# Performance work log

Measured on AMD Instinct MI355X. Metric: run time of the kernel, lower is better.

## Reference

```python
import jax, jax.numpy as jnp
from jax import lax
import numpy as np


def _conv3d(x, W, b, stride=1, pad=1):
    y = lax.conv_general_dilated(x, W, (stride,) * 3, [(pad, pad)] * 3,
                                 dimension_numbers=('NCDHW', 'OIDHW', 'NCDHW'))
    return y + b[None, :, None, None, None]


def _deconv3d(x, W, b):
    # PyTorch ConvTranspose3d(k=4, s=2, p=1) == conv with lhs_dilation=2,
    # per-side pad = k-1-p = 2, spatially flipped kernel; W is (Cin, Cout, 4,4,4).
    Wf = jnp.flip(W, axis=(2, 3, 4)).transpose(1, 0, 2, 3, 4)
    y = lax.conv_general_dilated(x, Wf, (1, 1, 1), [(2, 2)] * 3,
                                 lhs_dilation=(2, 2, 2),
                                 dimension_numbers=('NCDHW', 'OIDHW', 'NCDHW'))
    return y + b[None, :, None, None, None]


def _inorm(x, eps=1e-5):
    # InstanceNorm3d (affine=False): normalize per (B, C) over spatial dims
    m = jnp.mean(x, axis=(2, 3, 4), keepdims=True)
    v = jnp.var(x, axis=(2, 3, 4), keepdims=True)
    return (x - m) * lax.rsqrt(v + eps)


def _leaky(x):
    return jnp.where(x >= 0, x, 0.1 * x)


def _cblock(x, W, b, stride=1):
    return _leaky(_inorm(_conv3d(x, W, b, stride)))


def _cost_volume(f1, f2, r=2):
    # Faithful to the original pad/mul/crop loop:
    # cost[shift][p] = mean_c f1[c, p] * f2[c, p + shift], zero-padded OOB.
    B, C, D, H, W = f1.shape
    f2p = jnp.pad(f2, ((0, 0), (0, 0), (r, r), (r, r), (r, r)))
    cv = [jnp.mean(f1 * f2p[:, :, r + v:r + v + D, r + h:r + h + H, r + d:r + d + W], axis=1)
          for v in range(-r, r + 1)
          for h in range(-r, r + 1)
          for d in range(-r, r + 1)]
    return jnp.stack(cv, axis=1)  # (B, (2r+1)^3 = 125, D, H, W)


def _warp(img, flow):
    # SpatialTransformation: dense 3D warp, trilinear sample at grid + flow,
    # coordinates clamped to the volume border.
    B, C, D, H, W = img.shape
    gd, gh, gw = jnp.meshgrid(jnp.arange(D, dtype=img.dtype),
                              jnp.arange(H, dtype=img.dtype),
                              jnp.arange(W, dtype=img.dtype), indexing='ij')
    cd = jnp.clip(gd[None] + flow[:, 0], 0.0, D - 1.0)
    ch = jnp.clip(gh[None] + flow[:, 1], 0.0, H - 1.0)
    cw = jnp.clip(gw[None] + flow[:, 2], 0.0, W - 1.0)

    def samp_b(imb, d, h, w):
        return jax.vmap(lambda c: jax.scipy.ndimage.map_coordinates(
            c, [d, h, w], order=1, mode='nearest'))(imb)

    return jax.vmap(samp_b)(img, cd, ch, cw)


def _forward(atlas, target, W_ct, b_ct, W1a, b1a, W1aa, b1aa, W1b, b1b,
             W2a, b2a, W2aa, b2aa, W2b, b2b,
             W20, b20, Wpf2, bpf2, Wd2, bd2, Wuf2, buf2,
             W10, b10, Wpf1, bpf1, Wd1, bd1, Wuf1, buf1,
             W00, b00, Wpf0, bpf0, Wd0, bd0):
    # modality='CT' (shared CT encoder), G=True, contrastive=False path
    im2 = _cblock(atlas, W_ct, b_ct, stride=2)
    im1 = _cblock(target, W_ct, b_ct, stride=2)
    c11 = _cblock(_cblock(_cblock(im1, W1a, b1a, 2), W1aa, b1aa), W1b, b1b)
    c21 = _cblock(_cblock(_cblock(im2, W1a, b1a, 2), W1aa, b1aa), W1b, b1b)
    c12 = _cblock(_cblock(_cblock(c11, W2a, b2a, 2), W2aa, b2aa), W2b, b2b)
    c22 = _cblock(_cblock(_cblock(c21, W2a, b2a, 2), W2aa, b2aa), W2b, b2b)

    x = _leaky(_cost_volume(c12, c22))
    x = _cblock(x, W20, b20)
    flow2 = _conv3d(x, Wpf2, bpf2)
    up_flow2 = _deconv3d(flow2, Wd2, bd2)
    up_feat2 = _deconv3d(x, Wuf2, buf2)

    warp1 = _warp(c21, up_flow2)
    corr1 = _leaky(_cost_volume(c11, warp1))
    x = jnp.concatenate((corr1, c11, up_flow2, up_feat2), axis=1)  # 125+16+3+3=147
    x = _cblock(x, W10, b10)
    flow1 = _conv3d(x, Wpf1, bpf1)
    up_flow1 = _deconv3d(flow1, Wd1, bd1)
    up_feat1 = _deconv3d(x, Wuf1, buf1)

    warp0 = _warp(im2, up_flow1)
    corr0 = _leaky(_cost_volume(im1, warp0))
    x = jnp.concatenate((corr0, im1, up_flow1, up_feat1), axis=1)  # 125+4+3+64=196
    x = _cblock(x, W00, b00)
    flow0 = _conv3d(x, Wpf0, bpf0)
    flow = _deconv3d(flow0, Wd0, bd0)
    return flow, c22, c12


def setup_inputs() -> dict:
    ks = jax.random.split(jax.random.key(0), 24)

    def w(i, shape):
        fan_in = int(np.prod(shape[1:]))
        return jax.random.normal(ks[i], shape, jnp.float32) * np.float32(np.sqrt(2.0 / fan_in))

    z = lambda n: jnp.zeros((n,), jnp.float32)
    S = 128
    return {
        'atlas': jax.random.normal(ks[0], (1, 1, S, S, S), jnp.float32),
        'target': jax.random.normal(ks[1], (1, 1, S, S, S), jnp.float32),
        'W_ct': w(2, (4, 1, 3, 3, 3)), 'b_ct': z(4),
        'W1a': w(3, (16, 4, 3, 3, 3)), 'b1a': z(16),
        'W1aa': w(4, (16, 16, 3, 3, 3)), 'b1aa': z(16),
        'W1b': w(5, (16, 16, 3, 3, 3)), 'b1b': z(16),
        'W2a': w(6, (32, 16, 3, 3, 3)), 'b2a': z(32),
        'W2aa': w(7, (32, 32, 3, 3, 3)), 'b2aa': z(32),
        'W2b': w(8, (32, 32, 3, 3, 3)), 'b2b': z(32),
        'W20': w(9, (32, 125, 3, 3, 3)), 'b20': z(32),
        'Wpf2': w(10, (3, 32, 3, 3, 3)) * 0.1, 'bpf2': z(3),
        'Wd2': w(11, (3, 3, 4, 4, 4)), 'bd2': z(3),
        'Wuf2': w(12, (32, 3, 4, 4, 4)), 'buf2': z(3),
        'W10': w(13, (32, 147, 3, 3, 3)), 'b10': z(32),
        'Wpf1': w(14, (3, 32, 3, 3, 3)) * 0.1, 'bpf1': z(3),
        'Wd1': w(15, (3, 3, 4, 4, 4)), 'bd1': z(3),
        'Wuf1': w(16, (32, 64, 4, 4, 4)), 'buf1': z(64),
        'W00': w(17, (32, 196, 3, 3, 3)), 'b00': z(32),
        'Wpf0': w(18, (3, 32, 3, 3, 3)) * 0.1, 'bpf0': z(3),
        'Wd0': w(19, (3, 3, 4, 4, 4)), 'bd0': z(3),
    }


def reference(atlas, target, W_ct, b_ct, W1a, b1a, W1aa, b1aa, W1b, b1b,
              W2a, b2a, W2aa, b2aa, W2b, b2b,
              W20, b20, Wpf2, bpf2, Wd2, bd2, Wuf2, buf2,
              W10, b10, Wpf1, bpf1, Wd1, bd1, Wuf1, buf1,
              W00, b00, Wpf0, bpf0, Wd0, bd0):
    return _forward(atlas, target, W_ct, b_ct, W1a, b1a, W1aa, b1aa, W1b, b1b,
                    W2a, b2a, W2aa, b2aa, W2b, b2b,
                    W20, b20, Wpf2, bpf2, Wd2, bd2, Wuf2, buf2,
                    W10, b10, Wpf1, bpf1, Wd1, bd1, Wuf1, buf1,
                    W00, b00, Wpf0, bpf0, Wd0, bd0)
```

## Files before the change

kernel.cpp:

```cpp
#include <hip/hip_runtime.h>
#include <cstddef>
#include <cstdint>

#define DIVUP(a,b) (((a)+(b)-1)/(b))

typedef __attribute__((ext_vector_type(8))) short short8;
typedef __attribute__((ext_vector_type(4))) float f32x4;

__device__ __forceinline__ ushort f2bf(float f) {
    union { float f; uint32_t u; } v; v.f = f;
    uint32_t r = v.u + 0x7fffu + ((v.u >> 16) & 1u);
    return (ushort)(r >> 16);
}

struct SwzB { int x, y, z; };
__device__ __forceinline__ SwzB swz_block() {
    int gx = gridDim.x, gy = gridDim.y;
    int n = gx * gy * gridDim.z;
    int lin = blockIdx.x + gx * (blockIdx.y + gy * blockIdx.z);
    if ((n & 7) == 0)
        lin = (lin & 7) * (n >> 3) + (lin >> 3);
    SwzB s;
    s.x = lin % gx;
    int t = lin / gx;
    s.y = t % gy;
    s.z = t / gy;
    return s;
}

template<int COUT, int STRIDE>
__global__ __launch_bounds__(256)
void conv3x3_k(const float* __restrict__ in0, const float* __restrict__ in1,
               const float* __restrict__ wgt, const float* __restrict__ bias,
               float* __restrict__ out, float* __restrict__ stats,
               int Cin, int D, int H, int W, int nz, long out_bs, int st_bs)
{
    constexpr int TD = 4, TH = 8, TW = 8;
    constexpr int ID = 2 * TD + 1, IH = 2 * TH + 1, IW = 2 * TW + 1;
    __shared__ float tile[ID * IH * IW];
    const int b = blockIdx.z / nz, zb = blockIdx.z % nz;
    const float* in = b ? in1 : in0;
    out += (long)b * out_bs;
    if (stats) stats += 2 * st_bs * b;
    const int Do = D / STRIDE, Ho = H / STRIDE, Wo = W / STRIDE;
    const int tid = threadIdx.x;
    const int tw = tid & 7, th = (tid >> 3) & 7, td = tid >> 6;
    const int ow0 = blockIdx.x * TW, oh0 = blockIdx.y * TH, od0 = zb * TD;
    const int iw0 = ow0 * STRIDE - 1, ih0 = oh0 * STRIDE - 1, id0 = od0 * STRIDE - 1;
    const size_t HWs = (size_t)H * W;

    float acc[COUT];
#pragma unroll
    for (int i = 0; i < COUT; i++) acc[i] = 0.f;

    for (int c = 0; c < Cin; ++c) {
        const float* inc = in + (size_t)c * D * HWs;
        for (int i = tid; i < ID * IH * IW; i += 256) {
            int lw = i % IW, lh = (i / IW) % IH, ld = i / (IW * IH);
            int gw = iw0 + lw, gh = ih0 + lh, gd = id0 + ld;
            float v = 0.f;
            if ((unsigned)gw < (unsigned)W && (unsigned)gh < (unsigned)H &&
                (unsigned)gd < (unsigned)D)
                v = inc[(size_t)gd * HWs + (size_t)gh * W + gw];
            tile[i] = v;
        }
        __syncthreads();
        float r[27];
        const int bd = td * STRIDE, bh = th * STRIDE, bw = tw * STRIDE;
#pragma unroll
        for (int kd = 0; kd < 3; kd++)
#pragma unroll
            for (int kh = 0; kh < 3; kh++)
#pragma unroll
                for (int kw = 0; kw < 3; kw++)
                    r[kd * 9 + kh * 3 + kw] =
                        tile[(bd + kd) * (IH * IW) + (bh + kh) * IW + (bw + kw)];
#pragma unroll
        for (int oc = 0; oc < COUT; ++oc) {
            const float* wp = wgt + ((size_t)oc * Cin + c) * 27;
            float s = 0.f;
#pragma unroll
            for (int t = 0; t < 27; t++) s = fmaf(wp[t], r[t], s);
            acc[oc] += s;
        }
        __syncthreads();
    }
    const size_t So = (size_t)Do * Ho * Wo;
    const size_t sp = (size_t)(od0 + td) * Ho * Wo + (size_t)(oh0 + th) * Wo + (ow0 + tw);
#pragma unroll
    for (int oc = 0; oc < COUT; ++oc)
        out[(size_t)oc * So + sp] = acc[oc] + bias[oc];

    if (stats) {
        __syncthreads();
        float* sm = tile;
        const int wv = tid >> 6, l = tid & 63;
#pragma unroll
        for (int oc = 0; oc < COUT; ++oc) {
            float sv = acc[oc] + bias[oc];
            float sq = sv * sv;
#pragma unroll
            for (int o = 32; o > 0; o >>= 1) {
                sv += __shfl_down(sv, o, 64);
                sq += __shfl_down(sq, o, 64);
            }
            if (l == 0) { sm[(wv * COUT + oc) * 2] = sv; sm[(wv * COUT + oc) * 2 + 1] = sq; }
        }
        __syncthreads();
        if (tid < COUT) {
            float s = 0.f, s2 = 0.f;
#pragma unroll
            for (int w = 0; w < 4; ++w) {
                s += sm[(w * COUT + tid) * 2];
                s2 += sm[(w * COUT + tid) * 2 + 1];
            }
            atomicAdd(&stats[2 * tid], s);
            atomicAdd(&stats[2 * tid + 1], s2);
        }
    }
}

template<int CP, int NF, int STRIDE, int MW, int COUTR>
__global__ __launch_bounds__(MW * 64, (STRIDE == 1) ? 2 : 4)
void mconv_k(const ushort* __restrict__ xcl, const ushort* __restrict__ wp,
             const float* __restrict__ bias, float* __restrict__ outcf,
             float* __restrict__ stats, const ushort* __restrict__ zbuf,
             int D, int H, int W, int nz, long in_bs, long out_bs, int st_bs)
{
    constexpr int KC = CP / 32;
    constexpr int MF = (STRIDE == 1) ? 4 : 1;
    constexpr int TD = MW;
    constexpr int TWl = (STRIDE == 1) ? 8 : 4;
    constexpr int HD = (STRIDE == 1) ? TD + 2 : 2 * TD + 1;
    constexpr int HH = (STRIDE == 1) ? 10 : 9;
    constexpr int HWd = (STRIDE == 1) ? 10 : 9;
    constexpr int HALO = HD * HH * HWd;
    constexpr int NTH = MW * 64;
    constexpr int NIT = (HALO * 4 + NTH - 1) / NTH;
    constexpr int PITCH = (STRIDE == 1) ? 32 : 40;
    constexpr int LDSZ_H = (STRIDE == 1) ? NIT * NTH * 8 : HALO * 40;
    constexpr int NITW = (9 * NF * 512 + NTH * 8 - 1) / (NTH * 8);
    constexpr int LDSZ_W = NITW * NTH * 8;
    constexpr int LDS_TOT = (STRIDE == 1) ? LDSZ_H + 2 * LDSZ_W : LDSZ_H;
    __shared__ __align__(16) ushort lds[LDS_TOT];

    const int tid = threadIdx.x;
    const int wv = tid >> 6, l = tid & 63;
    const SwzB sb = swz_block();
    const int b = sb.z / nz, zb = sb.z % nz;
    xcl += (long)b * in_bs;
    outcf += (long)b * out_bs;
    if (stats) stats += 2 * st_bs * b;
    const int od0 = zb * TD, oh0 = sb.y * ((STRIDE == 1) ? 8 : 4),
              ow0 = sb.x * TWl;
    const int id0 = od0 * STRIDE - 1, ih0 = oh0 * STRIDE - 1, iw0 = ow0 * STRIDE - 1;

    f32x4 acc[MF][NF];
#pragma unroll
    for (int mf = 0; mf < MF; mf++)
#pragma unroll
        for (int nf = 0; nf < NF; nf++) acc[mf][nf] = f32x4{0.f, 0.f, 0.f, 0.f};

    auto woff = [&](int kc, int kd, int kh, int kw, int nf) -> size_t {
        return ((((size_t)(kc * 3 + kd) * 3 + kh) * 3 + kw) * NF + nf) << 9;
    };

    if constexpr (STRIDE == 1) {
        ushort* const hab = lds;
        ushort* const wbA = lds + LDSZ_H;
        ushort* const wbB = lds + LDSZ_H + LDSZ_W;

        auto hstage = [&](int kc) {
#pragma unroll
            for (int it = 0; it < NIT; ++it) {
                int idx = it * NTH + tid;
                int pt = idx >> 2, part = idx & 3;
                int lw = pt % HWd, lh = (pt / HWd) % HH, ld = pt / (HWd * HH);
                int gx = iw0 + lw, gy = ih0 + lh, gz = id0 + ld;
                const ushort* src = zbuf;
                if (pt < HALO && (unsigned)gx < (unsigned)W &&
                    (unsigned)gy < (unsigned)H && (unsigned)gz < (unsigned)D)
                    src = xcl + (size_t)((gz * H + gy) * W + gx) * CP + part * 8;
                __builtin_amdgcn_global_load_lds(
                    (const __attribute__((address_space(1))) uint32_t*)(src + kc * 32),
                    (__attribute__((address_space(3))) uint32_t*)
                        &hab[(size_t)(it * NTH + (wv << 6)) * 8],
                    16, 0, 0);
            }
        };
        auto wstage = [&](int kc, int kd, ushort* dst) {
#pragma unroll
            for (int it = 0; it < NITW; ++it) {
                int idx = it * NTH + tid;
                const ushort* src = (idx < 9 * NF * 64)
                    ? wp + ((size_t)(kc * 3 + kd) * 9 * NF * 512 + (size_t)idx * 8)
                    : zbuf;
                __builtin_amdgcn_global_load_lds(
                    (const __attribute__((address_space(1))) uint32_t*)src,
                    (__attribute__((address_space(3))) uint32_t*)
                        &dst[(size_t)(it * NTH + (wv << 6)) * 8],
                    16, 0, 0);
            }
        };
        auto compute = [&](int kd, const ushort* w) {
#pragma unroll
            for (int kw = 0; kw < 3; ++kw) {
                short8 af[9];
#pragma unroll
                for (int r = 0; r < 9; ++r)
                    af[r] = *reinterpret_cast<const short8*>(
                        &hab[((wv + kd) * (HH * HWd) +
                              (r + ((l >> 3) & 1)) * HWd + (l & 7) + kw) * PITCH +
                             ((l >> 4) << 3)]);
#pragma unroll
                for (int kh = 0; kh < 3; ++kh) {
                    short8 bf[NF];
#pragma unroll
                    for (int nf = 0; nf < NF; ++nf)
                        bf[nf] = *reinterpret_cast<const short8*>(
                            &w[(size_t)(((kh * 3 + kw) * NF) + nf) * 512 + (l << 3)]);
#pragma unroll
                    for (int mf = 0; mf < MF; ++mf)
#pragma unroll
                        for (int nf = 0; nf < NF; ++nf)
                            acc[mf][nf] = __builtin_amdgcn_mfma_f32_16x16x32_bf16(
                                af[2 * mf + kh], bf[nf], acc[mf][nf], 0, 0, 0);
                }
            }
        };

        for (int kc = 0; kc < KC; ++kc) {
            hstage(kc);
            wstage(kc, 0, wbA);
            __syncthreads();
            wstage(kc, 1, wbB);
            compute(0, wbA);
            __syncthreads();
            wstage(kc, 2, wbA);
            compute(1, wbB);
            __syncthreads();
            compute(2, wbA);
            __syncthreads();
        }
    } else {
        uint4 v[NIT];
        auto stage = [&](int kc) {
#pragma unroll
            for (int it = 0; it < NIT; ++it) {
                int idx = it * NTH + tid;
                uint4 t = {0u, 0u, 0u, 0u};
                if (idx < HALO * 4) {
                    int pt = idx >> 2, part = idx & 3;
                    int lw = pt % HWd, lh = (pt / HWd) % HH, ld = pt / (HWd * HH);
                    int gx = iw0 + lw, gy = ih0 + lh, gz = id0 + ld;
                    if ((unsigned)gx < (unsigned)W && (unsigned)gy < (unsigned)H &&
                        (unsigned)gz < (unsigned)D)
                        t = *reinterpret_cast<const uint4*>(
                            xcl + ((size_t)((gz * H + gy) * W + gx)) * CP + kc * 32 + part * 8);
                }
                v[it] = t;
            }
        };

        stage(0);
        for (int kc = 0; kc < KC; ++kc) {
            if (kc) __syncthreads();
#pragma unroll
            for (int it = 0; it < NIT; ++it) {
                int idx = it * NTH + tid;
                if (idx < HALO * 4)
                    *reinterpret_cast<uint4*>(&lds[(idx >> 2) * PITCH + (idx & 3) * 8]) = v[it];
            }
            __syncthreads();
            if (kc + 1 < KC) stage(kc + 1);
#pragma unroll
            for (int t = 0; t < 27; ++t) {
                const int kd = t / 9, kh = (t / 3) % 3, kw = t % 3;
                short8 bf[NF];
#pragma unroll
                for (int nf = 0; nf < NF; ++nf)
                    bf[nf] = *reinterpret_cast<const short8*>(
                        wp + woff(kc, kd, kh, kw, nf) + (l << 3));
                int bw = l & 3, bh = (l >> 2) & 3;
                int p_loc = (2 * wv + kd) * (HH * HWd) + (2 * bh + kh) * HWd + (2 * bw + kw);
                short8 afs = *reinterpret_cast<const short8*>(&lds[p_loc * PITCH + ((l >> 4) << 3)]);
#pragma unroll
                for (int nf = 0; nf < NF; ++nf)
                    acc[0][nf] = __builtin_amdgcn_mfma_f32_16x16x32_bf16(
                        afs, bf[nf], acc[0][nf], 0, 0, 0);
            }
        }
    }
    const int Do = D / STRIDE, Ho = H / STRIDE, Wo = W / STRIDE;
    const size_t So = (size_t)Do * Ho * Wo;
    float ps[NF], ps2[NF];
#pragma unroll
    for (int nf = 0; nf < NF; ++nf) { ps[nf] = 0.f; ps2[nf] = 0.f; }
#pragma unroll
    for (int nf = 0; nf < NF; ++nf) {
        int oc = nf * 16 + (l & 15);
        float bv = (oc < COUTR) ? bias[oc] : 0.f;
#pragma unroll
        for (int mf = 0; mf < MF; ++mf) {
#pragma unroll
            for (int r = 0; r < 4; ++r) {
                int q = ((l >> 4) << 2) + r;
                int bw, bh;
                if (STRIDE == 1) { bw = q & 7; bh = 2 * mf + (q >> 3); }
                else             { bw = q & 3; bh = (q >> 2) & 3; }
                int p = ((od0 + wv) * Ho + (oh0 + bh)) * Wo + (ow0 + bw);
                float val = acc[mf][nf][r] + bv;
                if (oc < COUTR) {
                    outcf[(size_t)oc * So + p] = val;
                    ps[nf] += val; ps2[nf] = fmaf(val, val, ps2[nf]);
                }
            }
        }
    }
    if (stats) {
        __syncthreads();
        float* sm = (float*)lds;
#pragma unroll
        for (int nf = 0; nf < NF; ++nf) {
            float s = ps[nf], s2 = ps2[nf];
            s += __shfl_down(s, 32, 64);  s2 += __shfl_down(s2, 32, 64);
            s += __shfl_down(s, 16, 64);  s2 += __shfl_down(s2, 16, 64);
            if (l < 16) {
                sm[((wv * NF + nf) * 16 + l) * 2] = s;
                sm[((wv * NF + nf) * 16 + l) * 2 + 1] = s2;
            }
        }
        __syncthreads();
        if (tid < NF * 16) {
            int nf = tid >> 4, c = tid & 15, oc = nf * 16 + c;
            if (oc < COUTR) {
                float s = 0.f, s2 = 0.f;
#pragma unroll
                for (int w = 0; w < MW; ++w) {
                    s += sm[((w * NF + nf) * 16 + c) * 2];
                    s2 += sm[((w * NF + nf) * 16 + c) * 2 + 1];
                }
                atomicAdd(&stats[2 * oc], s);
                atomicAdd(&stats[2 * oc + 1], s2);
            }
        }
    }
}

struct WTask { const float* src; void* dst; int kind, Cin, COUT, KC, coutr, base; };
struct WTab { WTask t[17]; int n; };

__global__ __launch_bounds__(256)
void wprep_k(WTab tab)
{
    int b = blockIdx.x, ti = 0;
    for (int i = 0; i < tab.n; ++i) if (b >= tab.t[i].base) ti = i;
    const WTask tk = tab.t[ti];
    int idx = (b - tk.base) * 256 + threadIdx.x;
    if (tk.kind == 0) {
        int NF = tk.COUT >> 4;
        int tot = 27 * tk.KC * NF * 512;
        if (idx >= tot) return;
        int j = idx & 7, l = (idx >> 3) & 63;
        int g = idx >> 9;
        int nf = g % NF; g /= NF;
        int kw = g % 3; g /= 3;
        int kh = g % 3; g /= 3;
        int kd = g % 3; int kc = g / 3;
        int t = kd * 9 + kh * 3 + kw;
        int oc = nf * 16 + (l & 15);
        int c = kc * 32 + ((l >> 4) << 3) + j;
        float v = (c < tk.Cin && oc < tk.coutr)
                      ? tk.src[((size_t)oc * tk.Cin + c) * 27 + t] : 0.f;
        ((ushort*)tk.dst)[idx] = f2bf(v);
    } else if (tk.kind == 1) {
        int NF = tk.KC;
        int tot = 8 * 8 * NF * 512;
        if (idx >= tot) return;
        int j = idx & 7, l = (idx >> 3) & 63;
        int g = idx >> 9;
        int nf = g % NF; g /= NF;
        int t = g % 8; int pp = g / 8;
        int oc = nf * 16 + (l & 15);
        int c = ((l >> 4) << 3) + j;
        int kd_ = (t >> 2) & 1, kh_ = (t >> 1) & 1, kw_ = t & 1;
        int pd = (pp >> 2) & 1, ph = (pp >> 1) & 1, pw = pp & 1;
        int kd = 3 - pd - 2 * kd_, kh = 3 - ph - 2 * kh_, kw = 3 - pw - 2 * kw_;
        float v = (oc < tk.COUT)
                      ? tk.src[(size_t)(c * tk.COUT + oc) * 64 + kd * 16 + kh * 4 + kw] : 0.f;
        ((ushort*)tk.dst)[idx] = f2bf(v);
    } else {
        int tot = tk.Cin * tk.COUT * 64;
        if (idx >= tot) return;
        int k = idx & 63; int oc = (idx >> 6) % tk.COUT; int c = (idx >> 6) / tk.COUT;
        ((float*)tk.dst)[((size_t)c * 64 + k) * tk.COUT + oc] = tk.src[idx];
    }
}

template<int NF>
__global__ __launch_bounds__(256)
void mdeconv_k(const ushort* __restrict__ xcl, const ushort* __restrict__ wpd,
               const float* __restrict__ bias, ushort* __restrict__ outcl,
               int c0, int CPo, int Si)
{
    constexpr int HD = 5, HH = 9, HWd = 9, HALO = HD * HH * HWd;
    constexpr int PITCH = 32;
    __shared__ __align__(16) ushort lds[HALO * PITCH];
    const int tid = threadIdx.x, wv = tid >> 6, l = tid & 63;
    const SwzB sb = swz_block();
    const int pp = sb.z & 7, tz = sb.z >> 3;
    const int pd = (pp >> 2) & 1, ph = (pp >> 1) & 1, pw = pp & 1;
    const int oz0 = tz * 4, oy0 = sb.y * 8, ox0 = sb.x * 8;
    const int iz0 = oz0 + pd - 1, iy0 = oy0 + ph - 1, ix0 = ox0 + pw - 1;

    for (int idx = tid; idx < HALO * 4; idx += 256) {
        int pt = idx >> 2, part = idx & 3;
        int lw = pt % HWd, lh = (pt / HWd) % HH, ld = pt / (HWd * HH);
        int gx = ix0 + lw, gy = iy0 + lh, gz = iz0 + ld;
        uint4 t = {0u, 0u, 0u, 0u};
        if ((unsigned)gx < (unsigned)Si && (unsigned)gy < (unsigned)Si &&
            (unsigned)gz < (unsigned)Si)
            t = *reinterpret_cast<const uint4*>(
                xcl + ((size_t)((gz * Si + gy) * Si + gx)) * 32 + part * 8);
        *reinterpret_cast<uint4*>(&lds[pt * PITCH + part * 8]) = t;
    }
    __syncthreads();

    f32x4 acc[4][NF];
#pragma unroll
    for (int mf = 0; mf < 4; mf++)
#pragma unroll
        for (int nf = 0; nf < NF; nf++) acc[mf][nf] = f32x4{0.f, 0.f, 0.f, 0.f};

#pragma unroll
    for (int kd = 0; kd < 2; ++kd) {
#pragma unroll
        for (int kw = 0; kw < 2; ++kw) {
            short8 af[8];
#pragma unroll
            for (int r = 0; r < 8; ++r)
                af[r] = *reinterpret_cast<const short8*>(
                    &lds[((wv + kd) * (HH * HWd) + (r + ((l >> 3) & 1)) * HWd +
                          (l & 7) + kw) * PITCH + ((l >> 4) << 3)]);
#pragma unroll
            for (int kh = 0; kh < 2; ++kh) {
                const int t = kd * 4 + kh * 2 + kw;
                short8 bf[NF];
#pragma unroll
                for (int nf = 0; nf < NF; ++nf)
                    bf[nf] = *reinterpret_cast<const short8*>(
                        wpd + (((size_t)(pp * 8 + t) * NF + nf) << 9) + (l << 3));
#pragma unroll
                for (int mf = 0; mf < 4; ++mf)
#pragma unroll
                    for (int nf = 0; nf < NF; ++nf)
                        acc[mf][nf] = __builtin_amdgcn_mfma_f32_16x16x32_bf16(
                            af[2 * mf + kh], bf[nf], acc[mf][nf], 0, 0, 0);
            }
        }
    }
    const int Do = 2 * Si;
#pragma unroll
    for (int nf = 0; nf < NF; ++nf) {
        int oc = nf * 16 + (l & 15);
        float bv = bias[oc];
#pragma unroll
        for (int mf = 0; mf < 4; ++mf) {
#pragma unroll
            for (int r = 0; r < 4; ++r) {
                int q = ((l >> 4) << 2) + r;
                int bw = q & 7, bh = 2 * mf + (q >> 3);
                int oD = 2 * (oz0 + wv) + pd, oH = 2 * (oy0 + bh) + ph, oW = 2 * (ox0 + bw) + pw;
                outcl[(size_t)((oD * Do + oH) * Do + oW) * CPo + c0 + oc] =
                    f2bf(acc[mf][nf][r] + bv);
            }
        }
    }
}

template<int CIN>
__global__ __launch_bounds__(256)
void dctn_k(const float* __restrict__ in, const float* __restrict__ wt,
            const float* __restrict__ bias, float* __restrict__ outcf,
            ushort* __restrict__ outcl, int c0, int CPo, int Si)
{
    const int Do = 2 * Si;
    const size_t So = (size_t)Do * Do * Do, ni = (size_t)Si * Si * Si;
    size_t p = (size_t)blockIdx.x * 256 + threadIdx.x;
    if (p >= So) return;
    int oxW = (int)(p % Do), oyH = (int)((p / Do) % Do), ozD = (int)(p / ((size_t)Do * Do));
    int pw = oxW & 1, ph = oyH & 1, pd = ozD & 1;
    int xb = oxW >> 1, yb = oyH >> 1, zb = ozD >> 1;
    float acc[3] = {0.f, 0.f, 0.f};
    for (int c = 0; c < CIN; ++c) {
        const float* inc = in + (size_t)c * ni;
        const float* wc = wt + (size_t)c * 64 * 3;
#pragma unroll
        for (int jd = 0; jd < 2; jd++) {
            int iz = zb + pd - jd; if ((unsigned)iz >= (unsigned)Si) continue;
            int kd = 1 - pd + 2 * jd;
#pragma unroll
            for (int jh = 0; jh < 2; jh++) {
                int iy = yb + ph - jh; if ((unsigned)iy >= (unsigned)Si) continue;
                int kh = 1 - ph + 2 * jh;
#pragma unroll
                for (int jw = 0; jw < 2; jw++) {
                    int ix = xb + pw - jw; if ((unsigned)ix >= (unsigned)Si) continue;
                    int kw = 1 - pw + 2 * jw;
                    float v = inc[((size_t)iz * Si + iy) * Si + ix];
                    const float* wr = wc + (size_t)((kd * 4 + kh) * 4 + kw) * 3;
                    acc[0] = fmaf(wr[0], v, acc[0]);
                    acc[1] = fmaf(wr[1], v, acc[1]);
                    acc[2] = fmaf(wr[2], v, acc[2]);
                }
            }
        }
    }
#pragma unroll
    for (int oc = 0; oc < 3; ++oc) {
        float o = acc[oc] + bias[oc];
        if (outcf) outcf[(size_t)oc * So + p] = o;
        if (outcl) outcl[p * CPo + c0 + oc] = f2bf(o);
    }
}

__global__ __launch_bounds__(256)
void inorm_apply_k(const float* __restrict__ x, const float* __restrict__ stats,
                   float* __restrict__ y, size_t S, float invS,
                   ushort* __restrict__ ycl, int CP, int Cper, long ycl_bs,
                   float* __restrict__ yclf, int CPf, int Cf)
{
    int c = blockIdx.y;
    float sum = stats[2 * c], ss = stats[2 * c + 1];
    float m = sum * invS;
    float r = rsqrtf(fmaxf(ss * invS - m * m, 0.f) + 1e-5f);
    size_t i = (size_t)blockIdx.x * 256 + threadIdx.x;
    if (i >= S) return;
    float v = (x[(size_t)c * S + i] - m) * r;
    v = v >= 0.f ? v : 0.1f * v;
    y[(size_t)c * S + i] = v;
    if (ycl) {
        int b = c / Cper, cl = c - b * Cper;
        ycl[(long)b * ycl_bs + (long)i * CP + cl] = f2bf(v);
    }
    if (yclf && c < Cf)
        yclf[i * (size_t)CPf + c] = v;
}

template<int C, int CP, int COPYC>
__global__ __launch_bounds__(256)
void costvolw_k(const float* __restrict__ f1, const float* __restrict__ f2,
                ushort* __restrict__ outcl, int D, int H, int W)
{
    const size_t S = (size_t)D * H * W;
    size_t p = (size_t)blockIdx.x * 4 + (threadIdx.x >> 6);
    if (p >= S) return;
    const int l = threadIdx.x & 63;
    int x = (int)(p % W); int y = (int)((p / W) % H); int z = (int)(p / ((size_t)W * H));
    float a[C];
#pragma unroll
    for (int c = 0; c < C; c++) a[c] = f1[(size_t)c * S + p];
    const float inv = 1.f / C;
    ushort* op = outcl + p * CP;
#pragma unroll
    for (int rep = 0; rep < 2; rep++) {
        int s = l + rep * 64;
        if (s < 125) {
            int v = s / 25 - 2, h = (s / 5) % 5 - 2, d = s % 5 - 2;
            int zz = z + v, yy = y + h, xx = x + d;
            float acc = 0.f;
            if ((unsigned)zz < (unsigned)D && (unsigned)yy < (unsigned)H &&
                (unsigned)xx < (unsigned)W) {
                size_t q = ((size_t)zz * H + yy) * (size_t)W + xx;
#pragma unroll
                for (int c = 0; c < C; c++) acc = fmaf(a[c], f2[(size_t)c * S + q], acc);
            }
            acc *= inv;
            op[s] = f2bf(acc >= 0.f ? acc : 0.1f * acc);
        }
    }
    if (COPYC && l < C)
        op[125 + l] = f2bf(f1[(size_t)l * S + p]);
}

template<int C, int CP, int NP>
__global__ __launch_bounds__(256)
void costvolcl_k(const float* __restrict__ f1cl, const float* __restrict__ f2cl,
                 ushort* __restrict__ outcl, int D, int H, int W)
{
    const size_t S = (size_t)D * H * W;
    size_t p0 = ((size_t)blockIdx.x * 4 + (threadIdx.x >> 6)) * NP;
    if (p0 >= S) return;
    const int l = threadIdx.x & 63;
    float a[NP][C];
#pragma unroll
    for (int pp = 0; pp < NP; pp++)
#pragma unroll
        for (int c4 = 0; c4 < C / 4; c4++) {
            float4 t = *reinterpret_cast<const float4*>(&f1cl[(p0 + pp) * C + c4 * 4]);
            a[pp][c4 * 4 + 0] = t.x; a[pp][c4 * 4 + 1] = t.y;
            a[pp][c4 * 4 + 2] = t.z; a[pp][c4 * 4 + 3] = t.w;
        }
    const float inv = 1.f / C;
#pragma unroll
    for (int rep = 0; rep < 2; rep++) {
        int s = l + rep * 64;
        int v = s / 25 - 2, h = (s / 5) % 5 - 2, d = s % 5 - 2;
        bool sv = s < 125;
#pragma unroll
        for (int pp = 0; pp < NP; pp++) {
            size_t p = p0 + pp;
            int x = (int)(p % W), y = (int)((p / W) % H), z = (int)(p / ((size_t)W * H));
            int zz = z + v, yy = y + h, xx = x + d;
            float acc = 0.f;
            if (sv && (unsigned)zz < (unsigned)D && (unsigned)yy < (unsigned)H &&
                (unsigned)xx < (unsigned)W) {
                size_t q = ((size_t)zz * H + yy) * (size_t)W + xx;
#pragma unroll
                for (int c4 = 0; c4 < C / 4; c4++) {
                    float4 b = *reinterpret_cast<const float4*>(&f2cl[q * C + c4 * 4]);
                    acc = fmaf(a[pp][c4 * 4 + 0], b.x, acc);
                    acc = fmaf(a[pp][c4 * 4 + 1], b.y, acc);
                    acc = fmaf(a[pp][c4 * 4 + 2], b.z, acc);
                    acc = fmaf(a[pp][c4 * 4 + 3], b.w, acc);
                }
            }
            if (sv) {
                acc *= inv;
                outcl[p * CP + s] = f2bf(acc >= 0.f ? acc : 0.1f * acc);
            }
        }
    }
    if (l < C) {
#pragma unroll
        for (int pp = 0; pp < NP; pp++)
            outcl[(p0 + pp) * CP + 125 + l] = f2bf(f1cl[(p0 + pp) * C + l]);
    }
}

template<int C>
__global__ __launch_bounds__(256)
void warpcl_k(const float* __restrict__ img, const float* __restrict__ flow,
              float* __restrict__ outcl, int D, int H, int W)
{
    const size_t S = (size_t)D * H * W;
    size_t p = (size_t)blockIdx.x * 256 + threadIdx.x;
    if (p >= S) return;
    int x = (int)(p % W); int y = (int)((p / W) % H); int z = (int)(p / ((size_t)W * H));
    float cd = fminf(fmaxf((float)z + flow[p], 0.f), (float)(D - 1));
    float ch = fminf(fmaxf((float)y + flow[S + p], 0.f), (float)(H - 1));
    float cw = fminf(fmaxf((float)x + flow[2 * S + p], 0.f), (float)(W - 1));
    int d0 = (int)cd, h0 = (int)ch, w0 = (int)cw;
    float fd = cd - d0, fh = ch - h0, fw = cw - w0;
    int d1 = min(d0 + 1, D - 1), h1 = min(h0 + 1, H - 1), w1 = min(w0 + 1, W - 1);
    size_t i000 = ((size_t)d0 * H + h0) * W + w0, i001 = ((size_t)d0 * H + h0) * W + w1;
    size_t i010 = ((size_t)d0 * H + h1) * W + w0, i011 = ((size_t)d0 * H + h1) * W + w1;
    size_t i100 = ((size_t)d1 * H + h0) * W + w0, i101 = ((size_t)d1 * H + h0) * W + w1;
    size_t i110 = ((size_t)d1 * H + h1) * W + w0, i111 = ((size_t)d1 * H + h1) * W + w1;
    float w000 = (1 - fd) * (1 - fh) * (1 - fw), w001 = (1 - fd) * (1 - fh) * fw;
    float w010 = (1 - fd) * fh * (1 - fw),       w011 = (1 - fd) * fh * fw;
    float w100 = fd * (1 - fh) * (1 - fw),       w101 = fd * (1 - fh) * fw;
    float w110 = fd * fh * (1 - fw),             w111 = fd * fh * fw;
#pragma unroll
    for (int c4 = 0; c4 < C / 4; c4++) {
        float4 r;
        float* rr = reinterpret_cast<float*>(&r);
#pragma unroll
        for (int j = 0; j < 4; j++) {
            const float* ic = img + (size_t)(c4 * 4 + j) * S;
            rr[j] = w000 * ic[i000] + w001 * ic[i001] + w010 * ic[i010] + w011 * ic[i011]
                  + w100 * ic[i100] + w101 * ic[i101] + w110 * ic[i110] + w111 * ic[i111];
        }
        *reinterpret_cast<float4*>(&outcl[p * C + c4 * 4]) = r;
    }
}

static void apply(hipStream_t st, float* x, int C, size_t S, const float* stats,
                  ushort* ycl, int CP, int Cper, long ycl_bs,
                  float* yclf = nullptr, int CPf = 0, int Cf = 0)
{
    dim3 g((unsigned)DIVUP(S, 256), C);
    inorm_apply_k<<<g, 256, 0, st>>>(x, stats, x, S, 1.0f / (float)S, ycl, CP, Cper, ycl_bs,
                                     yclf, CPf, Cf);
}

extern "C" void kernel_launch(void* const* d_in, const int* in_sizes, int n_in,
                              void* d_out, int out_size, void* d_ws, size_t ws_size,
                              hipStream_t st)
{
    (void)in_sizes; (void)n_in; (void)out_size; (void)ws_size;
    const float* atlas  = (const float*)d_in[0];
    const float* target = (const float*)d_in[1];
    const float *W_ct = (const float*)d_in[2],  *b_ct = (const float*)d_in[3];
    const float *W1a  = (const float*)d_in[4],  *b1a  = (const float*)d_in[5];
    const float *W1aa = (const float*)d_in[6],  *b1aa = (const float*)d_in[7];
    const float *W1b  = (const float*)d_in[8],  *b1b  = (const float*)d_in[9];
    const float *W2a  = (const float*)d_in[10], *b2a  = (const float*)d_in[11];
    const float *W2aa = (const float*)d_in[12], *b2aa = (const float*)d_in[13];
    const float *W2b  = (const float*)d_in[14], *b2b  = (const float*)d_in[15];
    const float *W20  = (const float*)d_in[16], *b20  = (const float*)d_in[17];
    const float *Wpf2 = (const float*)d_in[18], *bpf2 = (const float*)d_in[19];
    const float *Wd2  = (const float*)d_in[20], *bd2  = (const float*)d_in[21];
    const float *Wuf2 = (const float*)d_in[22], *buf2 = (const float*)d_in[23];
    const float *W10  = (const float*)d_in[24], *b10  = (const float*)d_in[25];
    const float *Wpf1 = (const float*)d_in[26], *bpf1 = (const float*)d_in[27];
    const float *Wd1  = (const float*)d_in[28], *bd1  = (const float*)d_in[29];
    const float *Wuf1 = (const float*)d_in[30], *buf1 = (const float*)d_in[31];
    const float *W00  = (const float*)d_in[32], *b00  = (const float*)d_in[33];
    const float *Wpf0 = (const float*)d_in[34], *bpf0 = (const float*)d_in[35];
    const float *Wd0  = (const float*)d_in[36], *bd0  = (const float*)d_in[37];

    const size_t S128 = 128u * 128 * 128, S64 = 64u * 64 * 64, S32 = 32u * 32 * 32, S16 = 16u * 16 * 16;

    char* base = (char*)d_ws;
    size_t off = 0;
    auto AF = [&](size_t n) { off = (off + 255) & ~(size_t)255; float* p = (float*)(base + off); off += n * 4; return p; };
    auto AH = [&](size_t n) { off = (off + 255) & ~(size_t)255; ushort* p = (ushort*)(base + off); off += n * 2; return p; };

    ushort* wp1aa = AH(13824); ushort* wp1b = AH(13824);
    ushort* wp2a  = AH(27648); ushort* wp2aa = AH(27648); ushort* wp2b = AH(27648);
    ushort* wp20  = AH(110592); ushort* wp10 = AH(138240); ushort* wp00 = AH(193536);
    ushort* wpf2  = AH(13824);  ushort* wpf1 = AH(13824);  ushort* wpf0 = AH(13824);
    ushort* wpd_uf1 = AH(131072);
    float* wt_uf2 = AF(6144);
    float* wt_d2  = AF(576);    float* wt_d1 = AF(576);    float* wt_d0 = AF(576);
    float* stats = AF(1024);
    ushort* zbuf = AH(1024);
    float* im12 = AF(8 * S64);
    float* im1 = im12; float* im2 = im12 + 4 * S64;
    float* im1clf = AF(4 * S64);
    float* warp0clf = AF(4 * S64);
    float* c11clf = AF(16 * S32);
    float* warp1clf = AF(16 * S32);
    float* A1   = AF(32 * S32); ushort* A1cl = AH(2 * S32 * 32);
    float* B1   = AF(32 * S32); ushort* B1cl = AH(2 * S32 * 32);
    float* c1121 = AF(32 * S32); ushort* c1121cl = AH(2 * S32 * 32);
    float* c11 = c1121; float* c21 = c1121 + 16 * S32;
    float* A2   = AF(64 * S16); ushort* A2cl = AH(2 * S16 * 32);
    float* B2   = AF(64 * S16); ushort* B2cl = AH(2 * S16 * 32);
    ushort* cv2cl = AH(S16 * 128);
    float* x20  = AF(32 * S16); ushort* x20cl = AH(S16 * 32);
    float* flow2 = AF(3 * S16); float* upflow2 = AF(3 * S32);
    ushort* x147cl = AH(S32 * 160);
    float* x10  = AF(32 * S32); ushort* x10cl = AH(S32 * 32);
    float* flow1 = AF(3 * S32); float* upflow1 = AF(3 * S64);
    ushort* x196cl = AH(S64 * 224);
    float* x00  = AF(32 * S64); float* flow0 = AF(3 * S64);

    ushort* x00cl = x196cl;

    float* outF = (float*)d_out;
    float* c22o = outF + 3 * S128;
    float* c12o = c22o + 32 * S16;

    const int ST_IM=0, ST_A1=8, ST_B1=40, ST_C1=72, ST_A2=104, ST_B2=168, ST_C2=232,
              ST_X20=296, ST_X10=328, ST_X00=360;
    auto SP = [&](int o) { return stats + 2 * o; };
    hipMemsetAsync(stats, 0, 4096, st);
    hipMemsetAsync(zbuf, 0, 2048, st);

    WTab tab; int nb = 0, ti = 0;
    auto addw = [&](const float* s, void* d, int kind, int Cin, int COUT, int KC, int coutr) {
        int tot = (kind == 0) ? 27 * KC * (COUT >> 4) * 512
                 : (kind == 1) ? 8 * 8 * KC * 512 : Cin * COUT * 64;
        tab.t[ti] = WTask{s, d, kind, Cin, COUT, KC, coutr, nb};
        nb += DIVUP(tot, 256); ti++;
    };
    addw(W1aa, wp1aa, 0, 16, 16, 1, 16);
    addw(W1b,  wp1b,  0, 16, 16, 1, 16);
    addw(W2a,  wp2a,  0, 16, 32, 1, 32);
    addw(W2aa, wp2aa, 0, 32, 32, 1, 32);
    addw(W2b,  wp2b,  0, 32, 32, 1, 32);
    addw(W20,  wp20,  0, 125, 32, 4, 32);
    addw(W10,  wp10,  0, 147, 32, 5, 32);
    addw(W00,  wp00,  0, 196, 32, 7, 32);
    addw(Wpf2, wpf2,  0, 32, 16, 1, 3);
    addw(Wpf1, wpf1,  0, 32, 16, 1, 3);
    addw(Wpf0, wpf0,  0, 32, 16, 1, 3);
    addw(Wuf1, wpd_uf1, 1, 32, 64, 4, 64);
    addw(Wuf2, wt_uf2, 2, 32, 3, 0, 3);
    addw(Wd2,  wt_d2,  2, 3, 3, 0, 3);
    addw(Wd1,  wt_d1,  2, 3, 3, 0, 3);
    addw(Wd0,  wt_d0,  2, 3, 3, 0, 3);
    tab.n = ti;
    wprep_k<<<nb, 256, 0, st>>>(tab);

    conv3x3_k<4, 2><<<dim3(8, 8, 32), 256, 0, st>>>(target, atlas, W_ct, b_ct, im12,
                                                    SP(ST_IM), 1, 128, 128, 128,
                                                    16, (long)(4 * S64), 4);
    apply(st, im12, 8, S64, SP(ST_IM), nullptr, 0, 4, 0, im1clf, 4, 4);

    conv3x3_k<16, 2><<<dim3(4, 4, 16), 256, 0, st>>>(im1, im2, W1a, b1a, A1,
                                                     SP(ST_A1), 4, 64, 64, 64,
                                                     8, (long)(16 * S32), 16);
    apply(st, A1, 32, S32, SP(ST_A1), A1cl, 32, 16, (long)(S32 * 32));
    mconv_k<32, 1, 1, 2, 16><<<dim3(4, 4, 32), 128, 0, st>>>(A1cl, wp1aa, b1aa, B1, SP(ST_B1),
        zbuf, 32, 32, 32, 16, (long)(S32 * 32), (long)(16 * S32), 16);
    apply(st, B1, 32, S32, SP(ST_B1), B1cl, 32, 16, (long)(S32 * 32));
    mconv_k<32, 1, 1, 2, 16><<<dim3(4, 4, 32), 128, 0, st>>>(B1cl, wp1b, b1b, c1121, SP(ST_C1),
        zbuf, 32, 32, 32, 16, (long)(S32 * 32), (long)(16 * S32), 16);
    apply(st, c1121, 32, S32, SP(ST_C1), c1121cl, 32, 16, (long)(S32 * 32), c11clf, 16, 16);

    mconv_k<32, 2, 2, 4, 32><<<dim3(4, 4, 8), 256, 0, st>>>(c1121cl, wp2a, b2a, A2, SP(ST_A2),
        zbuf, 32, 32, 32, 4, (long)(S32 * 32), (long)(32 * S16), 32);
    apply(st, A2, 64, S16, SP(ST_A2), A2cl, 32, 32, (long)(S16 * 32));
    mconv_k<32, 2, 1, 2, 32><<<dim3(2, 2, 16), 128, 0, st>>>(A2cl, wp2aa, b2aa, B2, SP(ST_B2),
        zbuf, 16, 16, 16, 8, (long)(S16 * 32), (long)(32 * S16), 32);
    apply(st, B2, 64, S16, SP(ST_B2), B2cl, 32, 32, (long)(S16 * 32));
    mconv_k<32, 2, 1, 2, 32><<<dim3(2, 2, 16), 128, 0, st>>>(B2cl, wp2b, b2b, c12o, SP(ST_C2),
        zbuf, 16, 16, 16, 8, (long)(S16 * 32), (long)(c22o - c12o), 32);
    apply(st, c12o, 32, S16, SP(ST_C2), nullptr, 0, 32, 0);
    apply(st, c22o, 32, S16, SP(ST_C2 + 32), nullptr, 0, 32, 0);

    costvolw_k<32, 128, 0><<<DIVUP(S16, 4), 256, 0, st>>>(c12o, c22o, cv2cl, 16, 16, 16);
    mconv_k<128, 2, 1, 2, 32><<<dim3(2, 2, 8), 128, 0, st>>>(cv2cl, wp20, b20, x20, SP(ST_X20),
        zbuf, 16, 16, 16, 8, 0, 0, 0);
    apply(st, x20, 32, S16, SP(ST_X20), x20cl, 32, 32, 0);
    mconv_k<32, 1, 1, 2, 3><<<dim3(2, 2, 8), 128, 0, st>>>(x20cl, wpf2, bpf2, flow2, nullptr,
        zbuf, 16, 16, 16, 8, 0, 0, 0);
    dctn_k<3><<<DIVUP(8 * S16, 256), 256, 0, st>>>(flow2, wt_d2, bd2, upflow2, x147cl, 141, 160, 16);
    dctn_k<32><<<DIVUP(8 * S16, 256), 256, 0, st>>>(x20, wt_uf2, buf2, nullptr, x147cl, 144, 160, 16);

    warpcl_k<16><<<DIVUP(S32, 256), 256, 0, st>>>(c21, upflow2, warp1clf, 32, 32, 32);
    costvolcl_k<16, 160, 2><<<(unsigned)(S32 / 8), 256, 0, st>>>(c11clf, warp1clf, x147cl,
                                                                 32, 32, 32);
    mconv_k<160, 2, 1, 2, 32><<<dim3(4, 4, 16), 128, 0, st>>>(x147cl, wp10, b10, x10, SP(ST_X10),
        zbuf, 32, 32, 32, 16, 0, 0, 0);
    apply(st, x10, 32, S32, SP(ST_X10), x10cl, 32, 32, 0);
    mconv_k<32, 1, 1, 2, 3><<<dim3(4, 4, 16), 128, 0, st>>>(x10cl, wpf1, bpf1, flow1, nullptr,
        zbuf, 32, 32, 32, 16, 0, 0, 0);
    dctn_k<3><<<DIVUP(8 * S32, 256), 256, 0, st>>>(flow1, wt_d1, bd1, upflow1, x196cl, 129, 224, 32);
    mdeconv_k<4><<<dim3(4, 4, 64), 256, 0, st>>>(x10cl, wpd_uf1, buf1, x196cl, 132, 224, 32);

    warpcl_k<4><<<DIVUP(S64, 256), 256, 0, st>>>(im2, upflow1, warp0clf, 64, 64, 64);
    costvolcl_k<4, 224, 4><<<(unsigned)(S64 / 16), 256, 0, st>>>(im1clf, warp0clf, x196cl,
                                                                 64, 64, 64);
    mconv_k<224, 2, 1, 4, 32><<<dim3(8, 8, 16), 256, 0, st>>>(x196cl, wp00, b00, x00, SP(ST_X00),
        zbuf, 64, 64, 64, 16, 0, 0, 0);
    apply(st, x00, 32, S64, SP(ST_X00), x00cl, 32, 32, 0);
    mconv_k<32, 1, 1, 4, 3><<<dim3(8, 8, 16), 256, 0, st>>>(x00cl, wpf0, bpf0, flow0, nullptr,
        zbuf, 64, 64, 64, 16, 0, 0, 0);
    dctn_k<3><<<DIVUP(S128, 256), 256, 0, st>>>(flow0, wt_d0, bd0, outF, nullptr, 0, 0, 64);
}
```

Baseline: 862.8 us.

## Prefetch next channel-chunk halo into registers during compute for multi-chunk convs

```diff
diff --git a/kernel.cpp b/kernel.cpp
--- a/kernel.cpp
+++ b/kernel.cpp
@@ -170,7 +170,48 @@
         ushort* const wbA = lds + LDSZ_H;
         ushort* const wbB = lds + LDSZ_H + LDSZ_W;
 
-        auto hstage = [&](int kc) {
+        auto wstage = [&](int kc, int kd, ushort* dst) {
+#pragma unroll
+            for (int it = 0; it < NITW; ++it) {
+                int idx = it * NTH + tid;
+                const ushort* src = (idx < 9 * NF * 64)
+                    ? wp + ((size_t)(kc * 3 + kd) * 9 * NF * 512 + (size_t)idx * 8)
+                    : zbuf;
+                __builtin_amdgcn_global_load_lds(
+                    (const __attribute__((address_space(1))) uint32_t*)src,
+                    (__attribute__((address_space(3))) uint32_t*)
+                        &dst[(size_t)(it * NTH + (wv << 6)) * 8],
+                    16, 0, 0);
+            }
+        };
+        auto compute = [&](int kd, const ushort* w) {
+#pragma unroll
+            for (int kw = 0; kw < 3; ++kw) {
+                short8 af[9];
+#pragma unroll
+                for (int r = 0; r < 9; ++r)
+                    af[r] = *reinterpret_cast<const short8*>(
+                        &hab[((wv + kd) * (HH * HWd) +
+                              (r + ((l >> 3) & 1)) * HWd + (l & 7) + kw) * PITCH +
+                             ((l >> 4) << 3)]);
+#pragma unroll
+                for (int kh = 0; kh < 3; ++kh) {
+                    short8 bf[NF];
+#pragma unroll
+                    for (int nf = 0; nf < NF; ++nf)
+                        bf[nf] = *reinterpret_cast<const short8*>(
+                            &w[(size_t)(((kh * 3 + kw) * NF) + nf) * 512 + (l << 3)]);
+#pragma unroll
+                    for (int mf = 0; mf < MF; ++mf)
+#pragma unroll
+                        for (int nf = 0; nf < NF; ++nf)
+                            acc[mf][nf] = __builtin_amdgcn_mfma_f32_16x16x32_bf16(
+                                af[2 * mf + kh], bf[nf], acc[mf][nf], 0, 0, 0);
+                }
+            }
+        };
+
+        if constexpr (KC == 1) {
 #pragma unroll
             for (int it = 0; it < NIT; ++it) {
                 int idx = it * NTH + tid;
@@ -182,65 +223,62 @@
                     (unsigned)gy < (unsigned)H && (unsigned)gz < (unsigned)D)
                     src = xcl + (size_t)((gz * H + gy) * W + gx) * CP + part * 8;
                 __builtin_amdgcn_global_load_lds(
-                    (const __attribute__((address_space(1))) uint32_t*)(src + kc * 32),
+                    (const __attribute__((address_space(1))) uint32_t*)src,
                     (__attribute__((address_space(3))) uint32_t*)
                         &hab[(size_t)(it * NTH + (wv << 6)) * 8],
                     16, 0, 0);
             }
-        };
-        auto wstage = [&](int kc, int kd, ushort* dst) {
-#pragma unroll
-            for (int it = 0; it < NITW; ++it) {
-                int idx = it * NTH + tid;
-                const ushort* src = (idx < 9 * NF * 64)
-                    ? wp + ((size_t)(kc * 3 + kd) * 9 * NF * 512 + (size_t)idx * 8)
-                    : zbuf;
-                __builtin_amdgcn_global_load_lds(
-                    (const __attribute__((address_space(1))) uint32_t*)src,
-                    (__attribute__((address_space(3))) uint32_t*)
-                        &dst[(size_t)(it * NTH + (wv << 6)) * 8],
-                    16, 0, 0);
-            }
-        };
-        auto compute = [&](int kd, const ushort* w) {
-#pragma unroll
-            for (int kw = 0; kw < 3; ++kw) {
-                short8 af[9];
-#pragma unroll
-                for (int r = 0; r < 9; ++r)
-                    af[r] = *reinterpret_cast<const short8*>(
-                        &hab[((wv + kd) * (HH * HWd) +
-                              (r + ((l >> 3) & 1)) * HWd + (l & 7) + kw) * PITCH +
-                             ((l >> 4) << 3)]);
-#pragma unroll
-                for (int kh = 0; kh < 3; ++kh) {
-                    short8 bf[NF];
-#pragma unroll
-                    for (int nf = 0; nf < NF; ++nf)
-                        bf[nf] = *reinterpret_cast<const short8*>(
-                            &w[(size_t)(((kh * 3 + kw) * NF) + nf) * 512 + (l << 3)]);
-#pragma unroll
-                    for (int mf = 0; mf < MF; ++mf)
-#pragma unroll
-                        for (int nf = 0; nf < NF; ++nf)
-                            acc[mf][nf] = __builtin_amdgcn_mfma_f32_16x16x32_bf16(
-                                af[2 * mf + kh], bf[nf], acc[mf][nf], 0, 0, 0);
-                }
-            }
-        };
-
-        for (int kc = 0; kc < KC; ++kc) {
-            hstage(kc);
-            wstage(kc, 0, wbA);
+            wstage(0, 0, wbA);
             __syncthreads();
-            wstage(kc, 1, wbB);
+            wstage(0, 1, wbB);
             compute(0, wbA);
             __syncthreads();
-            wstage(kc, 2, wbA);
+            wstage(0, 2, wbA);
             compute(1, wbB);
             __syncthreads();
             compute(2, wbA);
             __syncthreads();
+        } else {
+            uint4 v[NIT];
+            auto hfetch = [&](int kc, int lo, int hi) {
+#pragma unroll
+                for (int it = 0; it < NIT; ++it) {
+                    if (it < lo || it >= hi) continue;
+                    int idx = it * NTH + tid;
+                    int pt = idx >> 2, part = idx & 3;
+                    int lw = pt % HWd, lh = (pt / HWd) % HH, ld = pt / (HWd * HH);
+                    int gx = iw0 + lw, gy = ih0 + lh, gz = id0 + ld;
+                    uint4 t = {0u, 0u, 0u, 0u};
+                    if (pt < HALO && (unsigned)gx < (unsigned)W &&
+                        (unsigned)gy < (unsigned)H && (unsigned)gz < (unsigned)D)
+                        t = *reinterpret_cast<const uint4*>(
+                            xcl + (size_t)((gz * H + gy) * W + gx) * CP + kc * 32 + part * 8);
+                    v[it] = t;
+                }
+            };
+            auto hwrite = [&]() {
+#pragma unroll
+                for (int it = 0; it < NIT; ++it)
+                    *reinterpret_cast<uint4*>(&lds[(size_t)(it * NTH + tid) * 8]) = v[it];
+            };
+            constexpr int NH = NIT / 2;
+
+            hfetch(0, 0, NIT);
+            for (int kc = 0; kc < KC; ++kc) {
+                hwrite();
+                wstage(kc, 0, wbA);
+                __syncthreads();
+                if (kc + 1 < KC) hfetch(kc + 1, 0, NH);
+                wstage(kc, 1, wbB);
+                compute(0, wbA);
+                __syncthreads();
+                if (kc + 1 < KC) hfetch(kc + 1, NH, NIT);
+                wstage(kc, 2, wbA);
+                compute(1, wbB);
+                __syncthreads();
+                compute(2, wbA);
+                __syncthreads();
+            }
         }
     } else {
         uint4 v[NIT];
```

Result: slower. 1.049 ms (+21.6%).
